# Optimization experiments

Hardware: AMD Instinct MI355X
Metric: run time of the kernel (lower is better)

## Reference

```python
import jax, jax.numpy as jnp
import numpy as np

P = 16; N_SIDE = 14; N_PATCH = 196
ENC_DIM = 1024; ENC_DEPTH = 2; ENC_HEADS = 16; ENC_DH = 64
DEC_DIM = 512; DEC_DEPTH = 1; DEC_HEADS = 8; DEC_DH = 64
NUM_MASKED = int(0.75 * N_PATCH)  # 147


def _ln(x, s, b):
    m = jnp.mean(x, axis=-1, keepdims=True)
    v = jnp.var(x, axis=-1, keepdims=True)
    return (x - m) * jax.lax.rsqrt(v + 1e-5) * s + b


def _mha(x, Wqkv, Wo, heads, dh):
    B, N, _ = x.shape
    q, k, v = jnp.split(x @ Wqkv, 3, axis=-1)
    rs = lambda t: t.reshape(B, N, heads, dh).transpose(0, 2, 1, 3)
    q, k, v = rs(q), rs(k), rs(v)
    scores = jnp.einsum('bhqd,bhkd->bhqk', q, k) / jnp.sqrt(jnp.float32(dh))
    att = jax.nn.softmax(scores, axis=-1)
    o = jnp.einsum('bhqk,bhkd->bhqd', att, v).transpose(0, 2, 1, 3).reshape(B, N, heads * dh)
    return o @ Wo


def _transformer(x, params, depth, heads, dh, lnfs, lnfb):
    (ln1s, ln1b, Wqkv, Wo, ln2s, ln2b, W1, b1, W2, b2) = params
    for i in range(depth):
        x = x + _mha(_ln(x, ln1s[i], ln1b[i]), Wqkv[i], Wo[i], heads, dh)
        h = jax.nn.gelu(_ln(x, ln2s[i], ln2b[i]) @ W1[i] + b1[i])
        x = x + h @ W2[i] + b2[i]
    return _ln(x, lnfs, lnfb)


def setup_inputs() -> dict:
    key = jax.random.key(0)
    ks = jax.random.split(key, 24)
    B = 64
    w = lambda k, s: (jax.random.normal(k, s, jnp.float32) * 0.02)
    E, IE = ENC_DIM, ENC_HEADS * ENC_DH
    D, ID = DEC_DIM, DEC_HEADS * DEC_DH
    d = {}
    d['images'] = jax.random.normal(ks[0], (B, 224, 224, 3), jnp.float32)
    d['rand'] = jax.random.uniform(ks[1], (B, N_PATCH), dtype=jnp.float32)
    d['patch_W'] = w(ks[2], (P * P * 3, E)); d['patch_b'] = jnp.zeros((E,), jnp.float32)
    d['pos_emb'] = w(ks[3], (N_PATCH, E))
    d['enc_ln1s'] = jnp.ones((ENC_DEPTH, E), jnp.float32); d['enc_ln1b'] = jnp.zeros((ENC_DEPTH, E), jnp.float32)
    d['enc_Wqkv'] = w(ks[4], (ENC_DEPTH, E, 3 * IE)); d['enc_Wo'] = w(ks[5], (ENC_DEPTH, IE, E))
    d['enc_ln2s'] = jnp.ones((ENC_DEPTH, E), jnp.float32); d['enc_ln2b'] = jnp.zeros((ENC_DEPTH, E), jnp.float32)
    d['enc_W1'] = w(ks[6], (ENC_DEPTH, E, 4 * E)); d['enc_b1'] = jnp.zeros((ENC_DEPTH, 4 * E), jnp.float32)
    d['enc_W2'] = w(ks[7], (ENC_DEPTH, 4 * E, E)); d['enc_b2'] = jnp.zeros((ENC_DEPTH, E), jnp.float32)
    d['enc_lnfs'] = jnp.ones((E,), jnp.float32); d['enc_lnfb'] = jnp.zeros((E,), jnp.float32)
    d['e2d_W'] = w(ks[8], (E, D)); d['e2d_b'] = jnp.zeros((D,), jnp.float32)
    d['mask_token'] = w(ks[9], (D,))
    d['dec_pos'] = w(ks[10], (N_PATCH, D))
    d['dec_ln1s'] = jnp.ones((DEC_DEPTH, D), jnp.float32); d['dec_ln1b'] = jnp.zeros((DEC_DEPTH, D), jnp.float32)
    d['dec_Wqkv'] = w(ks[11], (DEC_DEPTH, D, 3 * ID)); d['dec_Wo'] = w(ks[12], (DEC_DEPTH, ID, D))
    d['dec_ln2s'] = jnp.ones((DEC_DEPTH, D), jnp.float32); d['dec_ln2b'] = jnp.zeros((DEC_DEPTH, D), jnp.float32)
    d['dec_W1'] = w(ks[13], (DEC_DEPTH, D, 4 * D)); d['dec_b1'] = jnp.zeros((DEC_DEPTH, 4 * D), jnp.float32)
    d['dec_W2'] = w(ks[14], (DEC_DEPTH, 4 * D, D)); d['dec_b2'] = jnp.zeros((DEC_DEPTH, D), jnp.float32)
    d['dec_lnfs'] = jnp.ones((D,), jnp.float32); d['dec_lnfb'] = jnp.zeros((D,), jnp.float32)
    d['pix_W'] = w(ks[15], (D, E)); d['pix_b'] = jnp.zeros((E,), jnp.float32)  # pixel_dim == encoder_dim per source
    return d


def reference(images, rand, patch_W, patch_b, pos_emb,
              enc_ln1s, enc_ln1b, enc_Wqkv, enc_Wo, enc_ln2s, enc_ln2b,
              enc_W1, enc_b1, enc_W2, enc_b2, enc_lnfs, enc_lnfb,
              e2d_W, e2d_b, mask_token, dec_pos,
              dec_ln1s, dec_ln1b, dec_Wqkv, dec_Wo, dec_ln2s, dec_ln2b,
              dec_W1, dec_b1, dec_W2, dec_b2, dec_lnfs, dec_lnfb,
              pix_W, pix_b):
    B = images.shape[0]
    # patch embed: [B,224,224,3] -> [B,196,768] -> [B,196,1024]
    x = images.reshape(B, N_SIDE, P, N_SIDE, P, 3).transpose(0, 1, 3, 2, 4, 5).reshape(B, N_PATCH, P * P * 3)
    patches = x @ patch_W + patch_b
    tokens = patches + pos_emb
    # random masking via argsort of uniform noise
    order = jnp.argsort(rand, axis=-1)
    m_idx = order[:, :NUM_MASKED]        # [B,147]
    u_idx = order[:, NUM_MASKED:]        # [B,49]
    unmasked = jnp.take_along_axis(tokens, u_idx[:, :, None], axis=1)
    enc_params = (enc_ln1s, enc_ln1b, enc_Wqkv, enc_Wo, enc_ln2s, enc_ln2b, enc_W1, enc_b1, enc_W2, enc_b2)
    encoded = _transformer(unmasked, enc_params, ENC_DEPTH, ENC_HEADS, ENC_DH, enc_lnfs, enc_lnfb)
    dec_tok = encoded @ e2d_W + e2d_b + dec_pos[u_idx]
    mask_toks = mask_token + dec_pos[m_idx]
    bidx = jnp.arange(B)[:, None]
    all_tok = jnp.zeros((B, N_PATCH, DEC_DIM), dec_tok.dtype)
    all_tok = all_tok.at[bidx, u_idx].set(dec_tok)
    all_tok = all_tok.at[bidx, m_idx].set(mask_toks)
    dec_params = (dec_ln1s, dec_ln1b, dec_Wqkv, dec_Wo, dec_ln2s, dec_ln2b, dec_W1, dec_b1, dec_W2, dec_b2)
    decoded = _transformer(all_tok, dec_params, DEC_DEPTH, DEC_HEADS, DEC_DH, dec_lnfs, dec_lnfb)
    pred = jnp.take_along_axis(decoded, m_idx[:, :, None], axis=1) @ pix_W + pix_b
    target = jnp.take_along_axis(patches, m_idx[:, :, None], axis=1)
    return jnp.mean((pred - target) ** 2)
```

## Files before the change

### kernel.cpp

```cpp
#include <hip/hip_runtime.h>

typedef __attribute__((ext_vector_type(8))) __bf16 bf16x8;
typedef __attribute__((ext_vector_type(4))) float f32x4;

#define OFF_PATCH 0ull
#define OFF_X     25690112ull
#define OFF_LN    51380224ull
#define OFF_QKV   64225280ull
#define OFF_HID   103022592ull
#define OFF_WP    154402816ull
#define OFF_ORD   214695936ull
#define OFF_PART  214746112ull

#define WP_PATCH   0ull
#define WP_ENC_QKV 786432ull
#define WP_ENC_WO  7077888ull
#define WP_ENC_W1  9175040ull
#define WP_ENC_W2  17563648ull
#define WP_E2D     25952256ull
#define WP_DEC_QKV 26476544ull
#define WP_DEC_WO  27262976ull
#define WP_DEC_W1  27525120ull
#define WP_DEC_W2  28573696ull
#define WP_PIX     29622272ull

#define OM_BF16 0
#define OM_F32  1
#define OM_ACC  2
#define OM_GELU 3

__device__ __forceinline__ float b2f(unsigned short u) {
    return __uint_as_float(((unsigned int)u) << 16);
}
__device__ __forceinline__ unsigned short f2b(float f) {
    unsigned int x = __float_as_uint(f);
    x += 0x7fffu + ((x >> 16) & 1u);
    return (unsigned short)(x >> 16);
}
__device__ __forceinline__ float gelu_f(float x) {
    float u2 = 1.5957691216057308f * x * (1.f + 0.044715f * x * x);
    return x / (1.f + __expf(-u2));
}
__device__ __forceinline__ void gload16(const void* g, void* l) {
    __builtin_amdgcn_global_load_lds((const __attribute__((address_space(1))) void*)g,
                                     (__attribute__((address_space(3))) void*)l, 16, 0, 0);
}

struct PackArgs {
    const float* src[15];
    unsigned long long dstOff[15];
    int K[15], N[15];
    int tileStart[16];
};
__global__ __launch_bounds__(256) void pack_all(PackArgs pa, unsigned short* __restrict__ wp) {
    __shared__ float tile[32][33];
    int t = blockIdx.x;
    int d = 0;
    while (d < 14 && t >= pa.tileStart[d + 1]) ++d;
    int local = t - pa.tileStart[d];
    int K = pa.K[d], N = pa.N[d];
    int ntn = N >> 5;
    int kt = (local / ntn) << 5, nt = (local % ntn) << 5;
    const float* in = pa.src[d];
    unsigned short* out = wp + pa.dstOff[d];
    int tx = threadIdx.x & 31, ty = threadIdx.x >> 5;
#pragma unroll
    for (int i = 0; i < 32; i += 8) tile[ty + i][tx] = in[(size_t)(kt + ty + i) * N + nt + tx];
    __syncthreads();
#pragma unroll
    for (int i = 0; i < 32; i += 8)
        out[(size_t)(nt + ty + i) * K + kt + tx] = f2b(tile[tx][ty + i]);
}

__global__ __launch_bounds__(256) void patchify_kernel(const float* __restrict__ img,
                                                       unsigned short* __restrict__ Xp) {
    const long long total = 12544ll * 768;
    for (long long e = (long long)blockIdx.x * 256 + threadIdx.x; e < total;
         e += (long long)gridDim.x * 256) {
        int row = (int)(e / 768), k = (int)(e % 768);
        int b = row / 196, pi = row % 196;
        int py = pi / 14, px = pi % 14;
        int r = k / 48, rem = k % 48;
        int c = rem / 3, ch = rem % 3;
        long long src = (((long long)(b * 224 + py * 16 + r)) * 224 + (px * 16 + c)) * 3 + ch;
        Xp[e] = f2b(img[src]);
    }
}

template <int BM, int OM, bool ATOMIC, bool GATHER>
__global__ __launch_bounds__((BM / 32) * 64) void gemm3(const unsigned short* __restrict__ A,
                                                        const unsigned short* __restrict__ Bt,
                                                        void* __restrict__ Cv,
                                                        const float* __restrict__ bias,
                                                        const int* __restrict__ gord,
                                                        int M, int N, int K, int Kc) {
    constexpr int WAVES = BM / 32;
    constexpr int BRW = 128 / WAVES;
    constexpr int NIB = BRW / 8;
    __shared__ __align__(16) unsigned short S[BM * 64 + 128 * 64];
    const int tid = threadIdx.x, wave = tid >> 6, lane = tid & 63;
    int nwg = gridDim.x * gridDim.y;
    int orig = blockIdx.y * gridDim.x + blockIdx.x;
    int q = nwg >> 3, r8 = nwg & 7, xcd = orig & 7, off = orig >> 3;
    int wg = (xcd < r8 ? xcd * (q + 1) : r8 * (q + 1) + (xcd - r8) * q) + off;
    const int brow = (wg / gridDim.x) * BM, bcol = (wg % gridDim.x) * 128;
    const int kBeg = blockIdx.z * Kc;
    const int fr = lane & 15, fq = lane >> 4;
    const int wr = (wave >> 1) * 64, wc = (wave & 1) * 64;
    const int lr = lane >> 3;
    const int sca = ((lane & 7) ^ lr) * 8;
    const unsigned short* Agp[4];
#pragma unroll
    for (int i = 0; i < 4; ++i) {
        int r = brow + wave * 32 + i * 8 + lr;
        if (r > M - 1) r = M - 1;
        if constexpr (GATHER) {
            int bb = r / 147, jj = r - bb * 147;
            r = bb * 196 + gord[bb * 196 + jj];
        }
        Agp[i] = A + (size_t)r * K + kBeg + sca;
    }
    const unsigned short* Bgp[NIB];
#pragma unroll
    for (int i = 0; i < NIB; ++i) {
        int r = bcol + wave * BRW + i * 8 + lr;
        Bgp[i] = Bt + (size_t)r * K + kBeg + sca;
    }

    f32x4 acc[4][4];
#pragma unroll
    for (int m = 0; m < 4; ++m)
#pragma unroll
        for (int n = 0; n < 4; ++n) acc[m][n] = (f32x4){0.f, 0.f, 0.f, 0.f};

    const char* lds = (const char*)S;
    const int sw = (fr & 7) << 4;
    const int a0 = (wr + fr) * 128 + ((fq * 16) ^ sw);
    const int b0 = BM * 128 + (wc + fr) * 128 + ((fq * 16) ^ sw);

    const int nt = Kc >> 6;
    for (int t = 0; t < nt; ++t) {
        __syncthreads();
        const int k0 = t << 6;
#pragma unroll
        for (int i = 0; i < 4; ++i)
            gload16(Agp[i] + k0, S + (wave * 32 + i * 8) * 64);
#pragma unroll
        for (int i = 0; i < NIB; ++i)
            gload16(Bgp[i] + k0, S + BM * 64 + (wave * BRW + i * 8) * 64);
        __syncthreads();
        __builtin_amdgcn_s_setprio(1);
#pragma unroll
        for (int kk = 0; kk < 2; ++kk) {
            const int kx = kk * 64;
            bf16x8 af[4], bf[4];
#pragma unroll
            for (int m = 0; m < 4; ++m)
                af[m] = *(const bf16x8*)(lds + ((a0 ^ kx) + m * 2048));
#pragma unroll
            for (int n = 0; n < 4; ++n)
                bf[n] = *(const bf16x8*)(lds + ((b0 ^ kx) + n * 2048));
#pragma unroll
            for (int m = 0; m < 4; ++m)
#pragma unroll
                for (int n = 0; n < 4; ++n)
                    acc[m][n] = __builtin_amdgcn_mfma_f32_16x16x32_bf16(af[m], bf[n],
                                                                       acc[m][n], 0, 0, 0);
        }
        __builtin_amdgcn_s_setprio(0);
    }

    const bool addBias = (bias != nullptr) && (kBeg == 0);
#pragma unroll
    for (int m = 0; m < 4; ++m) {
        int rb = brow + wr + m * 16 + fq * 4;
#pragma unroll
        for (int r = 0; r < 4; ++r) {
            int row = rb + r;
            if (row < M) {
#pragma unroll
                for (int n = 0; n < 4; ++n) {
                    int col = bcol + wc + n * 16 + fr;
                    float v = acc[m][n][r];
                    if (addBias) v += bias[col];
                    size_t o = (size_t)row * N + col;
                    if constexpr (ATOMIC) atomicAdd((float*)Cv + o, v);
                    else if constexpr (OM == OM_BF16) ((unsigned short*)Cv)[o] = f2b(v);
                    else if constexpr (OM == OM_F32) ((float*)Cv)[o] = v;
                    else if constexpr (OM == OM_ACC) ((float*)Cv)[o] += v;
                    else ((unsigned short*)Cv)[o] = f2b(gelu_f(v));
                }
            }
        }
    }
}

template <int N, int H, int NW>
__global__ __launch_bounds__(NW * 64) void attn_mfma(const unsigned short* __restrict__ qkv,
                                                     unsigned short* __restrict__ out) {
    constexpr int Npad = ((N + 31) / 32) * 32;
    constexpr int NT = Npad / 16;
    constexpr int KS = Npad / 32;
    constexpr int PS = Npad + 8;
    constexpr int SQ = 3 * H * 64, SO = H * 64;
    __shared__ __align__(16) unsigned short Kl[Npad * 64];
    __shared__ __align__(16) unsigned short Vt[64 * PS];
    __shared__ __align__(16) unsigned short Pl[NW * 16 * PS];
    const int b = blockIdx.x / H, h = blockIdx.x % H;
    const unsigned short* base = qkv + (size_t)b * N * SQ;
    const int qoff = h * 64, koff = (H + h) * 64, voff = (2 * H + h) * 64;
    const int tid = threadIdx.x, wave = tid >> 6, lane = tid & 63;
    const int fr = lane & 15, fq = lane >> 4;

    for (int idx = tid; idx < Npad * 8; idx += NW * 64) {
        int row = idx >> 3, ch = idx & 7;
        uint4 v = {0u, 0u, 0u, 0u};
        if (row < N) v = *(const uint4*)(base + (size_t)row * SQ + koff + ch * 8);
        *(uint4*)((char*)Kl + row * 128 + ((ch * 16) ^ ((row & 7) << 4))) = v;
    }
    for (int idx = tid; idx < Npad * 32; idx += NW * 64) {
        int key = idx >> 5, d2 = (idx & 31) * 2;
        unsigned int v = 0;
        if (key < N) v = *(const unsigned int*)(base + (size_t)key * SQ + voff + d2);
        Vt[d2 * PS + key] = (unsigned short)(v & 0xffffu);
        Vt[(d2 + 1) * PS + key] = (unsigned short)(v >> 16);
    }
    __syncthreads();

    unsigned short* pw = Pl + wave * 16 * PS;
    for (int qt = wave; qt < NT; qt += NW) {
        const int q0 = qt * 16;
        int qr = q0 + fr;
        if (qr > N - 1) qr = N - 1;
        const unsigned short* qp = base + (size_t)qr * SQ + qoff + fq * 8;
        bf16x8 aq0 = *(const bf16x8*)qp;
        bf16x8 aq1 = *(const bf16x8*)(qp + 32);
        f32x4 sa[NT];
#pragma unroll
        for (int ct = 0; ct < NT; ++ct) sa[ct] = (f32x4){0.f, 0.f, 0.f, 0.f};
#pragma unroll
        for (int ct = 0; ct < NT; ++ct) {
            const char* kb = (const char*)Kl + (ct * 16 + fr) * 128;
            bf16x8 kf0 = *(const bf16x8*)(kb + ((fq * 16) ^ ((fr & 7) << 4)));
            bf16x8 kf1 = *(const bf16x8*)(kb + ((64 + fq * 16) ^ ((fr & 7) << 4)));
            sa[ct] = __builtin_amdgcn_mfma_f32_16x16x32_bf16(aq0, kf0, sa[ct], 0, 0, 0);
            sa[ct] = __builtin_amdgcn_mfma_f32_16x16x32_bf16(aq1, kf1, sa[ct], 0, 0, 0);
        }
        float mrow[4] = {-3e38f, -3e38f, -3e38f, -3e38f};
#pragma unroll
        for (int ct = 0; ct < NT; ++ct) {
            bool ok = (ct * 16 + fr) < N;
#pragma unroll
            for (int r = 0; r < 4; ++r) {
                float s = ok ? sa[ct][r] * 0.125f : -3e38f;
                sa[ct][r] = s;
                mrow[r] = fmaxf(mrow[r], s);
            }
        }
#pragma unroll
        for (int off = 1; off <= 8; off <<= 1)
#pragma unroll
            for (int r = 0; r < 4; ++r) mrow[r] = fmaxf(mrow[r], __shfl_xor(mrow[r], off));
        float ssum[4] = {0.f, 0.f, 0.f, 0.f};
#pragma unroll
        for (int ct = 0; ct < NT; ++ct)
#pragma unroll
            for (int r = 0; r < 4; ++r) {
                float p = __expf(sa[ct][r] - mrow[r]);
                sa[ct][r] = p;
                ssum[r] += p;
            }
#pragma unroll
        for (int off = 1; off <= 8; off <<= 1)
#pragma unroll
            for (int r = 0; r < 4; ++r) ssum[r] += __shfl_xor(ssum[r], off);
#pragma unroll
        for (int ct = 0; ct < NT; ++ct)
#pragma unroll
            for (int r = 0; r < 4; ++r)
                pw[(fq * 4 + r) * PS + ct * 16 + fr] = f2b(sa[ct][r]);
        f32x4 oa[4];
#pragma unroll
        for (int vt = 0; vt < 4; ++vt) oa[vt] = (f32x4){0.f, 0.f, 0.f, 0.f};
#pragma unroll
        for (int ks = 0; ks < KS; ++ks) {
            bf16x8 pa = *(const bf16x8*)(pw + fr * PS + ks * 32 + fq * 8);
#pragma unroll
            for (int vt = 0; vt < 4; ++vt) {
                bf16x8 vf = *(const bf16x8*)(&Vt[(vt * 16 + fr) * PS + ks * 32 + fq * 8]);
                oa[vt] = __builtin_amdgcn_mfma_f32_16x16x32_bf16(pa, vf, oa[vt], 0, 0, 0);
            }
        }
        float inv[4];
#pragma unroll
        for (int r = 0; r < 4; ++r) inv[r] = 1.f / ssum[r];
#pragma unroll
        for (int vt = 0; vt < 4; ++vt)
#pragma unroll
            for (int r = 0; r < 4; ++r) {
                int q = q0 + fq * 4 + r;
                if (q < N)
                    out[((size_t)b * N + q) * SO + h * 64 + vt * 16 + fr] =
                        f2b(oa[vt][r] * inv[r]);
            }
    }
}

__global__ __launch_bounds__(256) void argsort_kernel(const float* __restrict__ rnd,
                                                      int* __restrict__ ord) {
    __shared__ float vals[196];
    int b = blockIdx.x, t = threadIdx.x;
    if (t < 196) vals[t] = rnd[b * 196 + t];
    __syncthreads();
    if (t < 196) {
        float v = vals[t];
        int rank = 0;
        for (int j = 0; j < 196; ++j) {
            float vj = vals[j];
            rank += (vj < v) || (vj == v && j < t);
        }
        ord[b * 196 + rank] = t;
    }
}

__global__ __launch_bounds__(256) void gather_unmasked(const unsigned short* __restrict__ patches,
                                                       const float* __restrict__ pos,
                                                       const int* __restrict__ ord,
                                                       float* __restrict__ xe) {
    int row = blockIdx.x;
    int b = row / 49, i = row % 49;
    int src = ord[b * 196 + 147 + i];
    const unsigned short* pr = patches + ((size_t)(b * 196 + src) << 10);
    const float* pe = pos + ((size_t)src << 10);
    float* o = xe + ((size_t)row << 10);
    int d = threadIdx.x * 4;
    ushort4 pv = *(const ushort4*)(pr + d);
    float4 p4 = *(const float4*)(pe + d);
    float4 r;
    r.x = b2f(pv.x) + p4.x; r.y = b2f(pv.y) + p4.y;
    r.z = b2f(pv.z) + p4.z; r.w = b2f(pv.w) + p4.w;
    *(float4*)(o + d) = r;
}

template <int L>
__global__ __launch_bounds__(256) void ln_kernel(const float* __restrict__ x,
                                                 unsigned short* __restrict__ y,
                                                 const float* __restrict__ sw,
                                                 const float* __restrict__ bw) {
    __shared__ float red[8];
    const int tid = threadIdx.x;
    const float* xr = x + (size_t)blockIdx.x * L;
    float sum = 0.f, sq = 0.f;
    for (int i = tid * 4; i < L; i += 1024) {
        float4 v = *(const float4*)(xr + i);
        sum += v.x + v.y + v.z + v.w;
        sq += v.x * v.x + v.y * v.y + v.z * v.z + v.w * v.w;
    }
    for (int off = 32; off; off >>= 1) {
        sum += __shfl_xor(sum, off);
        sq += __shfl_xor(sq, off);
    }
    int wave = tid >> 6, lane = tid & 63;
    if (lane == 0) { red[wave] = sum; red[4 + wave] = sq; }
    __syncthreads();
    float ts = red[0] + red[1] + red[2] + red[3];
    float tq = red[4] + red[5] + red[6] + red[7];
    float mean = ts / L;
    float inv = rsqrtf(tq / L - mean * mean + 1e-5f);
    unsigned short* yr = y + (size_t)blockIdx.x * L;
    for (int i = tid * 4; i < L; i += 1024) {
        float4 v = *(const float4*)(xr + i);
        float4 s4 = *(const float4*)(sw + i);
        float4 b4 = *(const float4*)(bw + i);
        ushort4 o;
        o.x = f2b((v.x - mean) * inv * s4.x + b4.x);
        o.y = f2b((v.y - mean) * inv * s4.y + b4.y);
        o.z = f2b((v.z - mean) * inv * s4.z + b4.z);
        o.w = f2b((v.w - mean) * inv * s4.w + b4.w);
        *(ushort4*)(yr + i) = o;
    }
}

__global__ __launch_bounds__(256) void scatter_tokens(const float* __restrict__ dec_tok,
                                                      const float* __restrict__ dec_pos,
                                                      const float* __restrict__ mask_tok,
                                                      const int* __restrict__ ord,
                                                      float* __restrict__ all_tok) {
    int e = blockIdx.x;
    int b = e / 196, i = e % 196;
    int idx = ord[e];
    float* o = all_tok + ((size_t)(b * 196 + idx)) * 512;
    const float* dp = dec_pos + (size_t)idx * 512;
    int d = threadIdx.x * 4;
    if (d < 512) {
        float4 dv = *(const float4*)(dp + d);
        float4 sv;
        if (i < 147) sv = *(const float4*)(mask_tok + d);
        else sv = *(const float4*)(dec_tok + ((size_t)(b * 49 + (i - 147))) * 512 + d);
        float4 r = {sv.x + dv.x, sv.y + dv.y, sv.z + dv.z, sv.w + dv.w};
        *(float4*)(o + d) = r;
    }
}

__global__ __launch_bounds__(256) void loss_partial(const float* __restrict__ pred,
                                                    const unsigned short* __restrict__ patches,
                                                    const int* __restrict__ ord,
                                                    float* __restrict__ part) {
    __shared__ float red[8];
    float local = 0.f;
    const long long total = 9633792ll;
    for (long long e = (long long)blockIdx.x * 256 + threadIdx.x; e < total; e += 4096ll * 256) {
        int r = (int)(e >> 10), d = (int)(e & 1023);
        int b = r / 147, j = r % 147;
        int idx = ord[b * 196 + j];
        float t = b2f(patches[(((size_t)(b * 196 + idx)) << 10) + d]);
        float df = pred[e] - t;
        local += df * df;
    }
    for (int off = 32; off; off >>= 1) local += __shfl_xor(local, off);
    int wave = threadIdx.x >> 6, lane = threadIdx.x & 63;
    if (lane == 0) red[wave] = local;
    __syncthreads();
    if (threadIdx.x == 0) part[blockIdx.x] = red[0] + red[1] + red[2] + red[3];
}

__global__ __launch_bounds__(256) void loss_final(const float* __restrict__ part,
                                                  float* __restrict__ out) {
    __shared__ float red[8];
    float local = 0.f;
    for (int i = threadIdx.x; i < 4096; i += 256) local += part[i];
    for (int off = 32; off; off >>= 1) local += __shfl_xor(local, off);
    int wave = threadIdx.x >> 6, lane = threadIdx.x & 63;
    if (lane == 0) red[wave] = local;
    __syncthreads();
    if (threadIdx.x == 0) out[0] = (red[0] + red[1] + red[2] + red[3]) / 9633792.0f;
}

extern "C" void kernel_launch(void* const* d_in, const int* in_sizes, int n_in, void* d_out,
                              int out_size, void* d_ws, size_t ws_size, hipStream_t stream) {
    const float* images = (const float*)d_in[0];
    const float* rnd = (const float*)d_in[1];
    const float* patch_W = (const float*)d_in[2];
    const float* patch_b = (const float*)d_in[3];
    const float* pos_emb = (const float*)d_in[4];
    const float* enc_ln1s = (const float*)d_in[5];
    const float* enc_ln1b = (const float*)d_in[6];
    const float* enc_Wqkv = (const float*)d_in[7];
    const float* enc_Wo = (const float*)d_in[8];
    const float* enc_ln2s = (const float*)d_in[9];
    const float* enc_ln2b = (const float*)d_in[10];
    const float* enc_W1 = (const float*)d_in[11];
    const float* enc_b1 = (const float*)d_in[12];
    const float* enc_W2 = (const float*)d_in[13];
    const float* enc_b2 = (const float*)d_in[14];
    const float* enc_lnfs = (const float*)d_in[15];
    const float* enc_lnfb = (const float*)d_in[16];
    const float* e2d_W = (const float*)d_in[17];
    const float* e2d_b = (const float*)d_in[18];
    const float* mask_tok = (const float*)d_in[19];
    const float* dec_pos = (const float*)d_in[20];
    const float* dec_ln1s = (const float*)d_in[21];
    const float* dec_ln1b = (const float*)d_in[22];
    const float* dec_Wqkv = (const float*)d_in[23];
    const float* dec_Wo = (const float*)d_in[24];
    const float* dec_ln2s = (const float*)d_in[25];
    const float* dec_ln2b = (const float*)d_in[26];
    const float* dec_W1 = (const float*)d_in[27];
    const float* dec_b1 = (const float*)d_in[28];
    const float* dec_W2 = (const float*)d_in[29];
    const float* dec_b2 = (const float*)d_in[30];
    const float* dec_lnfs = (const float*)d_in[31];
    const float* dec_lnfb = (const float*)d_in[32];
    const float* pix_W = (const float*)d_in[33];
    const float* pix_b = (const float*)d_in[34];

    char* ws = (char*)d_ws;
    unsigned short* patches = (unsigned short*)(ws + OFF_PATCH);
    float* Rx = (float*)(ws + OFF_X);
    unsigned short* Rln = (unsigned short*)(ws + OFF_LN);
    unsigned short* RqkvB = (unsigned short*)(ws + OFF_QKV);
    float* RqkvF = (float*)(ws + OFF_QKV);
    unsigned short* Rhid = (unsigned short*)(ws + OFF_HID);
    unsigned short* wp = (unsigned short*)(ws + OFF_WP);
    int* ord = (int*)(ws + OFF_ORD);
    float* part = (float*)(ws + OFF_PART);
    float* out = (float*)d_out;

    PackArgs pa;
    int nd = 0, tiles = 0;
    auto ADDP = [&](const float* src, unsigned long long wpo, int K, int N) {
        pa.src[nd] = src; pa.dstOff[nd] = wpo; pa.K[nd] = K; pa.N[nd] = N;
        pa.tileStart[nd] = tiles;
        tiles += (K >> 5) * (N >> 5);
        ++nd;
    };
    ADDP(patch_W, WP_PATCH, 768, 1024);
    for (int l = 0; l < 2; ++l) {
        ADDP(enc_Wqkv + (size_t)l * 1024 * 3072, WP_ENC_QKV + (size_t)l * 3145728, 1024, 3072);
        ADDP(enc_Wo + (size_t)l * 1024 * 1024, WP_ENC_WO + (size_t)l * 1048576, 1024, 1024);
        ADDP(enc_W1 + (size_t)l * 1024 * 4096, WP_ENC_W1 + (size_t)l * 4194304, 1024, 4096);
        ADDP(enc_W2 + (size_t)l * 4096 * 1024, WP_ENC_W2 + (size_t)l * 4194304, 4096, 1024);
    }
    ADDP(e2d_W, WP_E2D, 1024, 512);
    ADDP(dec_Wqkv, WP_DEC_QKV, 512, 1536);
    ADDP(dec_Wo, WP_DEC_WO, 512, 512);
    ADDP(dec_W1, WP_DEC_W1, 512, 2048);
    ADDP(dec_W2, WP_DEC_W2, 2048, 512);
    ADDP(pix_W, WP_PIX, 512, 1024);
    pa.tileStart[nd] = tiles;
    pack_all<<<tiles, 256, 0, stream>>>(pa, wp);

    auto GEMM = [&](int om, const unsigned short* A, size_t wpo, void* C, const float* bias,
                    int M, int N, int K, int S, bool small, const int* gord = nullptr) {
        const unsigned short* Bt = wp + wpo;
        int Kc = K / S;
        if (!small) {
            dim3 g(N / 128, (M + 255) / 256, S);
            if (gord) gemm3<256, OM_F32, false, true><<<g, 512, 0, stream>>>(A, Bt, C, bias, gord, M, N, K, Kc);
            else if (S > 1) gemm3<256, OM_ACC, true, false><<<g, 512, 0, stream>>>(A, Bt, C, bias, nullptr, M, N, K, Kc);
            else if (om == OM_BF16) gemm3<256, OM_BF16, false, false><<<g, 512, 0, stream>>>(A, Bt, C, bias, nullptr, M, N, K, Kc);
            else if (om == OM_F32) gemm3<256, OM_F32, false, false><<<g, 512, 0, stream>>>(A, Bt, C, bias, nullptr, M, N, K, Kc);
            else if (om == OM_ACC) gemm3<256, OM_ACC, false, false><<<g, 512, 0, stream>>>(A, Bt, C, bias, nullptr, M, N, K, Kc);
            else gemm3<256, OM_GELU, false, false><<<g, 512, 0, stream>>>(A, Bt, C, bias, nullptr, M, N, K, Kc);
        } else {
            dim3 g(N / 128, (M + 127) / 128, S);
            if (S > 1) gemm3<128, OM_ACC, true, false><<<g, 256, 0, stream>>>(A, Bt, C, bias, nullptr, M, N, K, Kc);
            else if (om == OM_F32) gemm3<128, OM_F32, false, false><<<g, 256, 0, stream>>>(A, Bt, C, bias, nullptr, M, N, K, Kc);
            else gemm3<128, OM_BF16, false, false><<<g, 256, 0, stream>>>(A, Bt, C, bias, nullptr, M, N, K, Kc);
        }
    };

    patchify_kernel<<<4096, 256, 0, stream>>>(images, Rhid);
    GEMM(OM_BF16, Rhid, WP_PATCH, patches, patch_b, 12544, 1024, 768, 1, false);
    argsort_kernel<<<64, 256, 0, stream>>>(rnd, ord);
    gather_unmasked<<<3136, 256, 0, stream>>>(patches, pos_emb, ord, Rx);

    for (int l = 0; l < 2; ++l) {
        ln_kernel<1024><<<3136, 256, 0, stream>>>(Rx, Rln, enc_ln1s + l * 1024,
                                                  enc_ln1b + l * 1024);
        GEMM(OM_BF16, Rln, WP_ENC_QKV + (size_t)l * 3145728, RqkvB, nullptr, 3136, 3072, 1024,
             1, false);
        attn_mfma<49, 16, 4><<<64 * 16, 256, 0, stream>>>(RqkvB, Rhid);
        GEMM(OM_ACC, Rhid, WP_ENC_WO + (size_t)l * 1048576, Rx, nullptr, 3136, 1024, 1024, 4,
             false);
        ln_kernel<1024><<<3136, 256, 0, stream>>>(Rx, Rln, enc_ln2s + l * 1024,
                                                  enc_ln2b + l * 1024);
        GEMM(OM_GELU, Rln, WP_ENC_W1 + (size_t)l * 4194304, Rhid, enc_b1 + l * 4096, 3136,
             4096, 1024, 1, false);
        GEMM(OM_ACC, Rhid, WP_ENC_W2 + (size_t)l * 4194304, Rx, enc_b2 + l * 1024, 3136, 1024,
             4096, 4, false);
    }
    ln_kernel<1024><<<3136, 256, 0, stream>>>(Rx, Rln, enc_lnfs, enc_lnfb);

    GEMM(OM_F32, Rln, WP_E2D, RqkvF, e2d_b, 3136, 512, 1024, 1, true);
    scatter_tokens<<<12544, 256, 0, stream>>>(RqkvF, dec_pos, mask_tok, ord, Rx);

    ln_kernel<512><<<12544, 256, 0, stream>>>(Rx, Rln, dec_ln1s, dec_ln1b);
    GEMM(OM_BF16, Rln, WP_DEC_QKV, RqkvB, nullptr, 12544, 1536, 512, 1, false);
    attn_mfma<196, 8, 8><<<64 * 8, 512, 0, stream>>>(RqkvB, Rhid);
    GEMM(OM_ACC, Rhid, WP_DEC_WO, Rx, nullptr, 12544, 512, 512, 2, false);
    ln_kernel<512><<<12544, 256, 0, stream>>>(Rx, Rln, dec_ln2s, dec_ln2b);
    GEMM(OM_GELU, Rln, WP_DEC_W1, Rhid, dec_b1, 12544, 2048, 512, 1, false);
    GEMM(OM_ACC, Rhid, WP_DEC_W2, Rx, dec_b2, 12544, 512, 2048, 2, false);
    ln_kernel<512><<<12544, 256, 0, stream>>>(Rx, Rln, dec_lnfs, dec_lnfb);

    GEMM(OM_F32, Rln, WP_PIX, RqkvF, pix_b, 9408, 1024, 512, 1, false, ord);
    loss_partial<<<4096, 256, 0, stream>>>(RqkvF, patches, ord, part);
    loss_final<<<1, 256, 0, stream>>>(part, out);
}
```

Measured before the change: 863.8 us.

## Load GEMM A operand directly to registers with double-buffered prefetch

Replaces the large-tile GEMM with a 128x128 kernel that reads A fragments straight from global memory into registers, double-buffered across K steps. Only B is staged through LDS, and raw barriers with explicit vmcnt waits let the next A load overlap the current MFMA work. The small-GEMM path becomes a separate kernel without split-K support. The risks are uncoalesced per-lane A loads, higher register pressure, and dropping the atomic split-K path for small GEMMs.

```diff
diff --git a/kernel.cpp b/kernel.cpp
--- a/kernel.cpp
+++ b/kernel.cpp
@@ -44,6 +44,11 @@
 __device__ __forceinline__ void gload16(const void* g, void* l) {
     __builtin_amdgcn_global_load_lds((const __attribute__((address_space(1))) void*)g,
                                      (__attribute__((address_space(3))) void*)l, 16, 0, 0);
+}
+__device__ __forceinline__ void fbar() {
+    asm volatile("" ::: "memory");
+    __builtin_amdgcn_s_barrier();
+    asm volatile("" ::: "memory");
 }
 
 struct PackArgs {
@@ -87,44 +92,41 @@
     }
 }
 
-template <int BM, int OM, bool ATOMIC, bool GATHER>
-__global__ __launch_bounds__((BM / 32) * 64) void gemm3(const unsigned short* __restrict__ A,
-                                                        const unsigned short* __restrict__ Bt,
-                                                        void* __restrict__ Cv,
-                                                        const float* __restrict__ bias,
-                                                        const int* __restrict__ gord,
-                                                        int M, int N, int K, int Kc) {
-    constexpr int WAVES = BM / 32;
-    constexpr int BRW = 128 / WAVES;
-    constexpr int NIB = BRW / 8;
-    __shared__ __align__(16) unsigned short S[BM * 64 + 128 * 64];
+template <int OM, bool ATOMIC, bool GATHER>
+__global__ __launch_bounds__(256) void gemmA(const unsigned short* __restrict__ A,
+                                             const unsigned short* __restrict__ Bt,
+                                             void* __restrict__ Cv,
+                                             const float* __restrict__ bias,
+                                             const int* __restrict__ gord,
+                                             int M, int N, int K, int Kc) {
+    __shared__ __align__(16) unsigned short Bs[128 * 64];
     const int tid = threadIdx.x, wave = tid >> 6, lane = tid & 63;
     int nwg = gridDim.x * gridDim.y;
     int orig = blockIdx.y * gridDim.x + blockIdx.x;
     int q = nwg >> 3, r8 = nwg & 7, xcd = orig & 7, off = orig >> 3;
     int wg = (xcd < r8 ? xcd * (q + 1) : r8 * (q + 1) + (xcd - r8) * q) + off;
-    const int brow = (wg / gridDim.x) * BM, bcol = (wg % gridDim.x) * 128;
+    const int brow = (wg / gridDim.x) * 128, bcol = (wg % gridDim.x) * 128;
     const int kBeg = blockIdx.z * Kc;
     const int fr = lane & 15, fq = lane >> 4;
     const int wr = (wave >> 1) * 64, wc = (wave & 1) * 64;
     const int lr = lane >> 3;
     const int sca = ((lane & 7) ^ lr) * 8;
-    const unsigned short* Agp[4];
+    const unsigned short* Bgp[4];
 #pragma unroll
     for (int i = 0; i < 4; ++i) {
-        int r = brow + wave * 32 + i * 8 + lr;
+        int r = bcol + wave * 32 + i * 8 + lr;
+        Bgp[i] = Bt + (size_t)r * K + kBeg + sca;
+    }
+    const unsigned short* Ap[4];
+#pragma unroll
+    for (int m = 0; m < 4; ++m) {
+        int r = brow + wr + m * 16 + fr;
         if (r > M - 1) r = M - 1;
         if constexpr (GATHER) {
             int bb = r / 147, jj = r - bb * 147;
             r = bb * 196 + gord[bb * 196 + jj];
         }
-        Agp[i] = A + (size_t)r * K + kBeg + sca;
-    }
-    const unsigned short* Bgp[NIB];
-#pragma unroll
-    for (int i = 0; i < NIB; ++i) {
-        int r = bcol + wave * BRW + i * 8 + lr;
-        Bgp[i] = Bt + (size_t)r * K + kBeg + sca;
+        Ap[m] = A + (size_t)r * K + kBeg + fq * 8;
     }
 
     f32x4 acc[4][4];
@@ -133,30 +135,30 @@
 #pragma unroll
         for (int n = 0; n < 4; ++n) acc[m][n] = (f32x4){0.f, 0.f, 0.f, 0.f};
 
-    const char* lds = (const char*)S;
+    const char* lds = (const char*)Bs;
     const int sw = (fr & 7) << 4;
-    const int a0 = (wr + fr) * 128 + ((fq * 16) ^ sw);
-    const int b0 = BM * 128 + (wc + fr) * 128 + ((fq * 16) ^ sw);
-
-    const int nt = Kc >> 6;
-    for (int t = 0; t < nt; ++t) {
-        __syncthreads();
-        const int k0 = t << 6;
+    const int b0 = (wc + fr) * 128 + ((fq * 16) ^ sw);
+
+    bf16x8 afA[4][2], afB[4][2];
+    auto loadA = [&](bf16x8(&af)[4][2], int t) {
+#pragma unroll
+        for (int m = 0; m < 4; ++m) {
+            const unsigned short* p = Ap[m] + (t << 6);
+            af[m][0] = *(const bf16x8*)p;
+            af[m][1] = *(const bf16x8*)(p + 32);
+        }
+    };
+    auto stB = [&](int t) {
 #pragma unroll
         for (int i = 0; i < 4; ++i)
-            gload16(Agp[i] + k0, S + (wave * 32 + i * 8) * 64);
-#pragma unroll
-        for (int i = 0; i < NIB; ++i)
-            gload16(Bgp[i] + k0, S + BM * 64 + (wave * BRW + i * 8) * 64);
-        __syncthreads();
+            gload16(Bgp[i] + (t << 6), Bs + (wave * 32 + i * 8) * 64);
+    };
+    auto compute = [&](bf16x8(&af)[4][2]) {
         __builtin_amdgcn_s_setprio(1);
 #pragma unroll
         for (int kk = 0; kk < 2; ++kk) {
             const int kx = kk * 64;
-            bf16x8 af[4], bf[4];
-#pragma unroll
-            for (int m = 0; m < 4; ++m)
-                af[m] = *(const bf16x8*)(lds + ((a0 ^ kx) + m * 2048));
+            bf16x8 bf[4];
 #pragma unroll
             for (int n = 0; n < 4; ++n)
                 bf[n] = *(const bf16x8*)(lds + ((b0 ^ kx) + n * 2048));
@@ -164,10 +166,31 @@
             for (int m = 0; m < 4; ++m)
 #pragma unroll
                 for (int n = 0; n < 4; ++n)
-                    acc[m][n] = __builtin_amdgcn_mfma_f32_16x16x32_bf16(af[m], bf[n],
+                    acc[m][n] = __builtin_amdgcn_mfma_f32_16x16x32_bf16(af[m][kk], bf[n],
                                                                        acc[m][n], 0, 0, 0);
         }
         __builtin_amdgcn_s_setprio(0);
+    };
+
+    const int nt = Kc >> 6;
+    loadA(afA, 0);
+    for (int t = 0; t < nt; t += 2) {
+        fbar();
+        stB(t);
+        loadA(afB, t + 1);
+        asm volatile("s_waitcnt vmcnt(8)" ::: "memory");
+        fbar();
+        compute(afA);
+        fbar();
+        stB(t + 1);
+        if (t + 2 < nt) {
+            loadA(afA, t + 2);
+            asm volatile("s_waitcnt vmcnt(8)" ::: "memory");
+        } else {
+            asm volatile("s_waitcnt vmcnt(0)" ::: "memory");
+        }
+        fbar();
+        compute(afB);
     }
 
     const bool addBias = (bias != nullptr) && (kBeg == 0);
@@ -189,6 +212,92 @@
                     else if constexpr (OM == OM_F32) ((float*)Cv)[o] = v;
                     else if constexpr (OM == OM_ACC) ((float*)Cv)[o] += v;
                     else ((unsigned short*)Cv)[o] = f2b(gelu_f(v));
+                }
+            }
+        }
+    }
+}
+
+template <int OM>
+__global__ __launch_bounds__(256) void gemm3s(const unsigned short* __restrict__ A,
+                                              const unsigned short* __restrict__ Bt,
+                                              void* __restrict__ Cv,
+                                              const float* __restrict__ bias,
+                                              int M, int N, int K) {
+    __shared__ __align__(16) unsigned short S[2 * 128 * 64];
+    const int tid = threadIdx.x, wave = tid >> 6, lane = tid & 63;
+    int nwg = gridDim.x * gridDim.y;
+    int orig = blockIdx.y * gridDim.x + blockIdx.x;
+    int q = nwg >> 3, r8 = nwg & 7, xcd = orig & 7, off = orig >> 3;
+    int wg = (xcd < r8 ? xcd * (q + 1) : r8 * (q + 1) + (xcd - r8) * q) + off;
+    const int brow = (wg / gridDim.x) * 128, bcol = (wg % gridDim.x) * 128;
+    const int fr = lane & 15, fq = lane >> 4;
+    const int wr = (wave >> 1) * 64, wc = (wave & 1) * 64;
+    const int lr = lane >> 3;
+    const int sca = ((lane & 7) ^ lr) * 8;
+    const unsigned short* Agp[4];
+#pragma unroll
+    for (int i = 0; i < 4; ++i) {
+        int r = brow + wave * 32 + i * 8 + lr;
+        if (r > M - 1) r = M - 1;
+        Agp[i] = A + (size_t)r * K + sca;
+    }
+    const unsigned short* Bgp[4];
+#pragma unroll
+    for (int i = 0; i < 4; ++i) {
+        int r = bcol + wave * 32 + i * 8 + lr;
+        Bgp[i] = Bt + (size_t)r * K + sca;
+    }
+    f32x4 acc[4][4];
+#pragma unroll
+    for (int m = 0; m < 4; ++m)
+#pragma unroll
+        for (int n = 0; n < 4; ++n) acc[m][n] = (f32x4){0.f, 0.f, 0.f, 0.f};
+    const char* lds = (const char*)S;
+    const int sw = (fr & 7) << 4;
+    const int a0 = (wr + fr) * 128 + ((fq * 16) ^ sw);
+    const int b0 = 16384 + (wc + fr) * 128 + ((fq * 16) ^ sw);
+    const int nt = K >> 6;
+    for (int t = 0; t < nt; ++t) {
+        __syncthreads();
+        const int k0 = t << 6;
+#pragma unroll
+        for (int i = 0; i < 4; ++i) {
+            gload16(Agp[i] + k0, S + (wave * 32 + i * 8) * 64);
+            gload16(Bgp[i] + k0, S + 128 * 64 + (wave * 32 + i * 8) * 64);
+        }
+        __syncthreads();
+#pragma unroll
+        for (int kk = 0; kk < 2; ++kk) {
+            const int kx = kk * 64;
+            bf16x8 af[4], bf[4];
+#pragma unroll
+            for (int m = 0; m < 4; ++m) af[m] = *(const bf16x8*)(lds + ((a0 ^ kx) + m * 2048));
+#pragma unroll
+            for (int n = 0; n < 4; ++n) bf[n] = *(const bf16x8*)(lds + ((b0 ^ kx) + n * 2048));
+#pragma unroll
+            for (int m = 0; m < 4; ++m)
+#pragma unroll
+                for (int n = 0; n < 4; ++n)
+                    acc[m][n] = __builtin_amdgcn_mfma_f32_16x16x32_bf16(af[m], bf[n],
+                                                                       acc[m][n], 0, 0, 0);
+        }
+    }
+#pragma unroll
+    for (int m = 0; m < 4; ++m) {
+        int rb = brow + wr + m * 16 + fq * 4;
+#pragma unroll
+        for (int r = 0; r < 4; ++r) {
+            int row = rb + r;
+            if (row < M) {
+#pragma unroll
+                for (int n = 0; n < 4; ++n) {
+                    int col = bcol + wc + n * 16 + fr;
+                    float v = acc[m][n][r];
+                    if (bias) v += bias[col];
+                    size_t o = (size_t)row * N + col;
+                    if constexpr (OM == OM_F32) ((float*)Cv)[o] = v;
+                    else ((unsigned short*)Cv)[o] = f2b(v);
                 }
             }
         }
@@ -515,18 +624,17 @@
         const unsigned short* Bt = wp + wpo;
         int Kc = K / S;
         if (!small) {
-            dim3 g(N / 128, (M + 255) / 256, S);
-            if (gord) gemm3<256, OM_F32, false, true><<<g, 512, 0, stream>>>(A, Bt, C, bias, gord, M, N, K, Kc);
-            else if (S > 1) gemm3<256, OM_ACC, true, false><<<g, 512, 0, stream>>>(A, Bt, C, bias, nullptr, M, N, K, Kc);
-            else if (om == OM_BF16) gemm3<256, OM_BF16, false, false><<<g, 512, 0, stream>>>(A, Bt, C, bias, nullptr, M, N, K, Kc);
-            else if (om == OM_F32) gemm3<256, OM_F32, false, false><<<g, 512, 0, stream>>>(A, Bt, C, bias, nullptr, M, N, K, Kc);
-            else if (om == OM_ACC) gemm3<256, OM_ACC, false, false><<<g, 512, 0, stream>>>(A, Bt, C, bias, nullptr, M, N, K, Kc);
-            else gemm3<256, OM_GELU, false, false><<<g, 512, 0, stream>>>(A, Bt, C, bias, nullptr, M, N, K, Kc);
+            dim3 g(N / 128, (M + 127) / 128, S);
+            if (gord) gemmA<OM_F32, false, true><<<g, 256, 0, stream>>>(A, Bt, C, bias, gord, M, N, K, Kc);
+            else if (S > 1) gemmA<OM_ACC, true, false><<<g, 256, 0, stream>>>(A, Bt, C, bias, nullptr, M, N, K, Kc);
+            else if (om == OM_BF16) gemmA<OM_BF16, false, false><<<g, 256, 0, stream>>>(A, Bt, C, bias, nullptr, M, N, K, Kc);
+            else if (om == OM_F32) gemmA<OM_F32, false, false><<<g, 256, 0, stream>>>(A, Bt, C, bias, nullptr, M, N, K, Kc);
+            else if (om == OM_ACC) gemmA<OM_ACC, false, false><<<g, 256, 0, stream>>>(A, Bt, C, bias, nullptr, M, N, K, Kc);
+            else gemmA<OM_GELU, false, false><<<g, 256, 0, stream>>>(A, Bt, C, bias, nullptr, M, N, K, Kc);
         } else {
-            dim3 g(N / 128, (M + 127) / 128, S);
-            if (S > 1) gemm3<128, OM_ACC, true, false><<<g, 256, 0, stream>>>(A, Bt, C, bias, nullptr, M, N, K, Kc);
-            else if (om == OM_F32) gemm3<128, OM_F32, false, false><<<g, 256, 0, stream>>>(A, Bt, C, bias, nullptr, M, N, K, Kc);
-            else gemm3<128, OM_BF16, false, false><<<g, 256, 0, stream>>>(A, Bt, C, bias, nullptr, M, N, K, Kc);
+            dim3 g(N / 128, (M + 127) / 128, 1);
+            if (om == OM_F32) gemm3s<OM_F32><<<g, 256, 0, stream>>>(A, Bt, C, bias, M, N, K);
+            else gemm3s<OM_BF16><<<g, 256, 0, stream>>>(A, Bt, C, bias, M, N, K);
         }
     };
 
```

Result: slower. 1.266 ms (+46.6%).
